# Optimization experiments

Measured on AMD Instinct MI355X. Metric: run time of the kernel, lower is better.

Reference implementation:

```python
import jax, jax.numpy as jnp
import numpy as np

HEAD = 16
EMB = 1024
D_K = EMB // HEAD


def setup_inputs() -> dict:
    key = jax.random.key(0)
    ks = jax.random.split(key, 11)
    B, S, E = 2, 2048, EMB
    scale = 1.0 / np.sqrt(E)
    inp = {
        "query": jax.random.normal(ks[0], (B, S, E), jnp.float32),
        "key": jax.random.normal(ks[1], (B, S, E), jnp.float32),
        "value": jax.random.normal(ks[2], (B, S, E), jnp.float32),
        "Wq": jax.random.normal(ks[3], (E, E), jnp.float32) * scale,
        "bq": jnp.zeros((E,), jnp.float32),
        "Wk": jax.random.normal(ks[4], (E, E), jnp.float32) * scale,
        "bk": jnp.zeros((E,), jnp.float32),
        "Wv": jax.random.normal(ks[5], (E, E), jnp.float32) * scale,
        "bv": jnp.zeros((E,), jnp.float32),
        "Wo": jax.random.normal(ks[6], (E, E), jnp.float32) * scale,
        "bo": jnp.zeros((E,), jnp.float32),
    }
    return inp


def reference(query, key, value, Wq, bq, Wk, bk, Wv, bv, Wo, bo):
    B, S, E = query.shape
    # 3 input projections, split into heads: [B, H, S, d_k]
    def proj(x, W, b):
        return (x @ W.T + b).reshape(B, S, HEAD, D_K).transpose(0, 2, 1, 3)

    q = proj(query, Wq, bq)
    k = proj(key, Wk, bk)
    v = proj(value, Wv, bv)

    # scaled dot-product attention (full matrix, as in original)
    scores = jnp.einsum("bhqd,bhkd->bhqk", q, k) / jnp.sqrt(jnp.float32(D_K))
    attn = jax.nn.softmax(scores, axis=-1)  # dropout in eval mode = identity
    x = jnp.einsum("bhqk,bhkd->bhqd", attn, v)

    # merge heads and output projection
    x = x.transpose(0, 2, 1, 3).reshape(B, S, E)
    return x @ Wo.T + bo
```

## Files before the change

kernel.cpp:

```cpp
#include <hip/hip_runtime.h>
#include <hip/hip_bf16.h>
#include <math.h>


constexpr int Sn = 2048;
constexpr int En = 1024;
constexpr int Hn = 16;
constexpr int Dk = 64;
constexpr int Kn = 1024;
constexpr size_t WSZ = 1048576;
constexpr size_t TSZ = 4194304;

#define QSCALE 0.18033688011112042f

typedef __bf16 bf16x8 __attribute__((ext_vector_type(8)));
typedef float  f32x4  __attribute__((ext_vector_type(4)));
typedef float  f32x16 __attribute__((ext_vector_type(16)));

union U16 { uint4 u; bf16x8 v; __hip_bfloat16 h[8]; };
union U8  { uint2 u; __hip_bfloat162 h2[2]; __hip_bfloat16 h[4]; };
union U4  { unsigned u; __hip_bfloat162 h2; };

__device__ inline U16 cvt8f(const float* __restrict__ p) {
    float4 a = *(const float4*)p;
    float4 b = *(const float4*)(p + 4);
    U16 r;
    r.h[0] = __float2bfloat16(a.x); r.h[1] = __float2bfloat16(a.y);
    r.h[2] = __float2bfloat16(a.z); r.h[3] = __float2bfloat16(a.w);
    r.h[4] = __float2bfloat16(b.x); r.h[5] = __float2bfloat16(b.y);
    r.h[6] = __float2bfloat16(b.z); r.h[7] = __float2bfloat16(b.w);
    return r;
}

__device__ inline void gload16(const __hip_bfloat16* g, __hip_bfloat16* l) {
    __builtin_amdgcn_global_load_lds(
        (const __attribute__((address_space(1))) void*)g,
        (__attribute__((address_space(3))) void*)l, 16, 0, 0);
}

template<int ROWS, int NW>
__device__ inline void stage_tile(const __hip_bfloat16* __restrict__ src, int ld,
                                  __hip_bfloat16* lds, int w, int lane) {
    int l8 = lane >> 3;
    int g = (lane & 7) ^ (l8 & 7);
    #pragma unroll
    for (int j = 0; j < ROWS / (8 * NW); ++j) {
        int c = j * NW + w;
        gload16(src + (size_t)(c * 8 + l8) * ld + g * 8, lds + c * 512);
    }
}

__global__ __launch_bounds__(256)
void cvt_w(const float* __restrict__ w0, const float* __restrict__ w1,
           const float* __restrict__ w2, const float* __restrict__ w3,
           __hip_bfloat16* __restrict__ dst)
{
    int y = blockIdx.y;
    const float* src = (y == 0) ? w0 : (y == 1) ? w1 : (y == 2) ? w2 : w3;
    size_t i = ((size_t)blockIdx.x * 256 + threadIdx.x) * 8;
    U16 r = cvt8f(src + i);
    *(uint4*)&dst[(size_t)y * WSZ + i] = r.u;
}

__global__ __launch_bounds__(256)
void cvt_x3(const float* __restrict__ q, const float* __restrict__ k,
            const float* __restrict__ v, __hip_bfloat16* __restrict__ dst)
{
    int z = blockIdx.y;
    const float* src = (z == 0) ? q : (z == 1) ? k : v;
    size_t i = ((size_t)blockIdx.x * 256 + threadIdx.x) * 8;
    U16 r = cvt8f(src + i);
    *(uint4*)&dst[(size_t)z * TSZ + i] = r.u;
}

template<int NT>
__device__ inline void gemm_core(const __hip_bfloat16* __restrict__ Ab,
                                 const __hip_bfloat16* __restrict__ Wb,
                                 __hip_bfloat16* As, __hip_bfloat16* Bs,
                                 f32x4 (&acc)[2][NT], int w, int lane)
{
    const int l15 = lane & 15, lg = lane >> 4, l7 = lane & 7;
    const int wm = (w & 1) * 32, wn = (w >> 1) * (NT * 16);
    const int coff0 = (lg ^ l7) * 8;
    const int coff1 = ((4 + lg) ^ l7) * 8;

    #pragma unroll
    for (int i = 0; i < 2; ++i)
        #pragma unroll
        for (int j = 0; j < NT; ++j) acc[i][j] = {0.f, 0.f, 0.f, 0.f};

    for (int k0 = 0; k0 < Kn; k0 += 64) {
        stage_tile<64, 4>(Ab + k0, Kn, As, w, lane);
        stage_tile<NT * 32, 4>(Wb + k0, Kn, Bs, w, lane);
        __syncthreads();

        U16 af[2][2], bf[NT][2];
        #pragma unroll
        for (int mt = 0; mt < 2; ++mt) {
            int r = (wm + mt * 16 + l15) * 64;
            af[mt][0].u = *(const uint4*)&As[r + coff0];
            af[mt][1].u = *(const uint4*)&As[r + coff1];
        }
        #pragma unroll
        for (int nt = 0; nt < NT; ++nt) {
            int r = (wn + nt * 16 + l15) * 64;
            bf[nt][0].u = *(const uint4*)&Bs[r + coff0];
            bf[nt][1].u = *(const uint4*)&Bs[r + coff1];
        }
        #pragma unroll
        for (int mt = 0; mt < 2; ++mt)
            #pragma unroll
            for (int nt = 0; nt < NT; ++nt) {
                acc[mt][nt] = __builtin_amdgcn_mfma_f32_16x16x32_bf16(af[mt][0].v, bf[nt][0].v, acc[mt][nt], 0, 0, 0);
                acc[mt][nt] = __builtin_amdgcn_mfma_f32_16x16x32_bf16(af[mt][1].v, bf[nt][1].v, acc[mt][nt], 0, 0, 0);
            }
        __syncthreads();
    }
}

__global__ __launch_bounds__(256)
void gemm_qkv(const __hip_bfloat16* __restrict__ X, const __hip_bfloat16* __restrict__ Wall,
              const float* __restrict__ bq, const float* __restrict__ bk,
              const float* __restrict__ bv, __hip_bfloat16* __restrict__ outbase)
{
    __shared__ __align__(16) __hip_bfloat16 As[64 * 64];
    __shared__ __align__(16) __hip_bfloat16 Bs[128 * 64];

    const int tid = threadIdx.x, w = tid >> 6, lane = tid & 63;
    const int z = blockIdx.z;
    const int blockM = blockIdx.x * 64, blockN = blockIdx.y * 128;

    f32x4 acc[2][4];
    gemm_core<4>(X + (size_t)z * TSZ + (size_t)blockM * Kn,
                 Wall + (size_t)z * WSZ + (size_t)blockN * Kn,
                 As, Bs, acc, w, lane);

    const float scale = (z == 0) ? QSCALE : 1.0f;
    const float* bias = (z == 0) ? bq : (z == 1) ? bk : bv;
    __hip_bfloat16* out = outbase + (size_t)z * TSZ;

    const int l15 = lane & 15, lg = lane >> 4;
    const int wm = (w & 1) * 32, wn = (w >> 1) * 64;

    #pragma unroll
    for (int nt = 0; nt < 4; ++nt) {
        int n = blockN + wn + nt * 16 + l15;
        float bvn = bias[n] * scale;
        int h_ = n >> 6, d_ = n & 63;
        #pragma unroll
        for (int mt = 0; mt < 2; ++mt) {
            int m0 = blockM + wm + mt * 16 + lg * 4;
            int b_ = m0 >> 11, s_ = m0 & (Sn - 1);
            if (z < 2) {
                #pragma unroll
                for (int i = 0; i < 4; ++i)
                    out[(((size_t)b_ * Hn + h_) * Sn + s_ + i) * Dk + d_] =
                        __float2bfloat16(fmaf(acc[mt][nt][i], scale, bvn));
            } else {
                U8 pk;
                #pragma unroll
                for (int i = 0; i < 4; ++i)
                    pk.h[i] = __float2bfloat16(fmaf(acc[mt][nt][i], scale, bvn));
                *(uint2*)&out[(((size_t)b_ * Hn + h_) * Dk + d_) * Sn + s_] = pk.u;
            }
        }
    }
}

__global__ __launch_bounds__(256)
void gemm_out(const __hip_bfloat16* __restrict__ A, const __hip_bfloat16* __restrict__ W,
              const float* __restrict__ bias, float* __restrict__ out)
{
    __shared__ __align__(16) __hip_bfloat16 As[64 * 64];
    __shared__ __align__(16) __hip_bfloat16 Bs[64 * 64];

    const int tid = threadIdx.x, w = tid >> 6, lane = tid & 63;
    const int blockM = blockIdx.x * 64, blockN = blockIdx.y * 64;

    f32x4 acc[2][2];
    gemm_core<2>(A + (size_t)blockM * Kn, W + (size_t)blockN * Kn,
                 As, Bs, acc, w, lane);

    const int l15 = lane & 15, lg = lane >> 4;
    const int wm = (w & 1) * 32, wn = (w >> 1) * 32;

    #pragma unroll
    for (int nt = 0; nt < 2; ++nt) {
        int n = blockN + wn + nt * 16 + l15;
        float bvn = bias[n];
        #pragma unroll
        for (int mt = 0; mt < 2; ++mt) {
            int m0 = blockM + wm + mt * 16 + lg * 4;
            #pragma unroll
            for (int i = 0; i < 4; ++i)
                out[(size_t)(m0 + i) * Kn + n] = acc[mt][nt][i] + bvn;
        }
    }
}

__global__ __launch_bounds__(256)
void attn(const __hip_bfloat16* __restrict__ Q, const __hip_bfloat16* __restrict__ K,
          const __hip_bfloat16* __restrict__ Vt, __hip_bfloat16* __restrict__ X)
{
    __shared__ __align__(16) __hip_bfloat16 Ks[4][64 * 64];
    __shared__ __align__(16) __hip_bfloat16 Vts[4][64 * 64];

    const int bh = blockIdx.y, q0 = blockIdx.x * 128;
    const int tid = threadIdx.x, w = tid >> 6, lane = tid & 63;
    const int l31 = lane & 31, hi = lane >> 5;

    const __hip_bfloat16* Qb = Q  + (size_t)bh * Sn * Dk;
    const __hip_bfloat16* Kb = K  + (size_t)bh * Sn * Dk;
    const __hip_bfloat16* Vb = Vt + (size_t)bh * Dk * Sn;

    U16 qf[4];
    {
        const __hip_bfloat16* qp = Qb + (size_t)(q0 + w * 32 + l31) * Dk + hi * 8;
        #pragma unroll
        for (int d0t = 0; d0t < 4; ++d0t)
            qf[d0t].u = *(const uint4*)(qp + d0t * 16);
    }
    asm volatile("s_waitcnt vmcnt(0)" ::: "memory");

    f32x16 o[2];
    #pragma unroll
    for (int dt = 0; dt < 2; ++dt)
        #pragma unroll
        for (int r = 0; r < 16; ++r) o[dt][r] = 0.f;
    float lpart = 0.f;

    #pragma unroll
    for (int p = 0; p < 3; ++p) {
        stage_tile<64, 4>(Kb + (size_t)p * 64 * Dk, Dk, Ks[p], w, lane);
        stage_tile<64, 4>(Vb + p * 64, Sn, Vts[p], w, lane);
    }

    for (int t = 0; t < Sn / 64; ++t) {
        asm volatile("s_waitcnt vmcnt(8)" ::: "memory");
        __builtin_amdgcn_s_barrier();
        __builtin_amdgcn_sched_barrier(0);

        const int ts = (t + 3) & 31;
        const int sb = (t + 3) & 3;
        stage_tile<64, 4>(Kb + (size_t)ts * 64 * Dk, Dk, Ks[sb], w, lane);
        stage_tile<64, 4>(Vb + ts * 64, Sn, Vts[sb], w, lane);

        const int cur = t & 3;

        f32x16 st[2];
        #pragma unroll
        for (int kt = 0; kt < 2; ++kt)
            #pragma unroll
            for (int r = 0; r < 16; ++r) st[kt][r] = 0.f;

        __builtin_amdgcn_s_setprio(1);
        #pragma unroll
        for (int d0t = 0; d0t < 4; ++d0t) {
            #pragma unroll
            for (int kt = 0; kt < 2; ++kt) {
                int r = kt * 32 + l31;
                int col = (((d0t * 2 + hi)) ^ (r & 7)) * 8;
                U16 kf; kf.u = *(const uint4*)&Ks[cur][r * 64 + col];
                st[kt] = __builtin_amdgcn_mfma_f32_32x32x16_bf16(kf.v, qf[d0t].v, st[kt], 0, 0, 0);
            }
        }
        __builtin_amdgcn_s_setprio(0);

        uint4 pa[4];
        #pragma unroll
        for (int kt = 0; kt < 2; ++kt) {
            float pv[16];
            #pragma unroll
            for (int r = 0; r < 16; ++r) pv[r] = __builtin_amdgcn_exp2f(st[kt][r]);
            float s01 = (pv[0] + pv[1]) + (pv[2] + pv[3]);
            float s23 = (pv[4] + pv[5]) + (pv[6] + pv[7]);
            float s45 = (pv[8] + pv[9]) + (pv[10] + pv[11]);
            float s67 = (pv[12] + pv[13]) + (pv[14] + pv[15]);
            lpart += (s01 + s23) + (s45 + s67);

            uint wv[8];
            #pragma unroll
            for (int m2 = 0; m2 < 8; ++m2) {
                U4 pk; pk.h2 = __float22bfloat162_rn({pv[2 * m2], pv[2 * m2 + 1]});
                wv[m2] = pk.u;
            }
            asm volatile("v_permlane32_swap_b32 %0, %1" : "+v"(wv[0]), "+v"(wv[2]));
            asm volatile("v_permlane32_swap_b32 %0, %1" : "+v"(wv[1]), "+v"(wv[3]));
            asm volatile("v_permlane32_swap_b32 %0, %1" : "+v"(wv[4]), "+v"(wv[6]));
            asm volatile("v_permlane32_swap_b32 %0, %1" : "+v"(wv[5]), "+v"(wv[7]));
            pa[kt * 2 + 0] = make_uint4(wv[0], wv[1], wv[2], wv[3]);
            pa[kt * 2 + 1] = make_uint4(wv[4], wv[5], wv[6], wv[7]);
        }

        __builtin_amdgcn_s_setprio(1);
        #pragma unroll
        for (int k0t = 0; k0t < 4; ++k0t) {
            U16 pau; pau.u = pa[k0t];
            #pragma unroll
            for (int dt = 0; dt < 2; ++dt) {
                int r = dt * 32 + l31;
                int col = (((k0t * 2 + hi)) ^ (r & 7)) * 8;
                U16 vf; vf.u = *(const uint4*)&Vts[cur][r * 64 + col];
                o[dt] = __builtin_amdgcn_mfma_f32_32x32x16_bf16(pau.v, vf.v, o[dt], 0, 0, 0);
            }
        }
        __builtin_amdgcn_s_setprio(0);
    }

    asm volatile("s_waitcnt vmcnt(0)" ::: "memory");

    lpart += __shfl_xor(lpart, 32, 64);
    float linv = 1.f / lpart;

    float li[16];
    #pragma unroll
    for (int r = 0; r < 16; ++r) {
        int qr = (r & 3) + 8 * (r >> 2) + 4 * hi;
        li[r] = __shfl(linv, qr, 64);
    }

    int b_ = bh >> 4, h_ = bh & (Hn - 1);
    #pragma unroll
    for (int r = 0; r < 16; ++r) {
        int qr = (r & 3) + 8 * (r >> 2) + 4 * hi;
        int sr = q0 + w * 32 + qr;
        __hip_bfloat16* xp = X + ((size_t)(b_ * Sn + sr)) * En + h_ * Dk + l31;
        xp[0]  = __float2bfloat16(o[0][r] * li[r]);
        xp[32] = __float2bfloat16(o[1][r] * li[r]);
    }
}

extern "C" void kernel_launch(void* const* d_in, const int* in_sizes, int n_in,
                              void* d_out, int out_size, void* d_ws, size_t ws_size,
                              hipStream_t stream)
{
    const float* query = (const float*)d_in[0];
    const float* key   = (const float*)d_in[1];
    const float* value = (const float*)d_in[2];
    const float* Wq = (const float*)d_in[3];
    const float* bq = (const float*)d_in[4];
    const float* Wk = (const float*)d_in[5];
    const float* bk = (const float*)d_in[6];
    const float* Wv = (const float*)d_in[7];
    const float* bv = (const float*)d_in[8];
    const float* Wo = (const float*)d_in[9];
    const float* bo = (const float*)d_in[10];
    float* out = (float*)d_out;

    __hip_bfloat16* xqkv = (__hip_bfloat16*)d_ws;
    __hip_bfloat16* Wbf  = xqkv + 3 * TSZ;
    __hip_bfloat16* QKVw = Wbf + 4 * WSZ;
    __hip_bfloat16* Xw   = xqkv;

    cvt_w<<<dim3(512, 4), 256, 0, stream>>>(Wq, Wk, Wv, Wo, Wbf);
    cvt_x3<<<dim3(2048, 3), 256, 0, stream>>>(query, key, value, xqkv);
    gemm_qkv<<<dim3(64, 8, 3), 256, 0, stream>>>(xqkv, Wbf, bq, bk, bv, QKVw);
    attn<<<dim3(Sn / 128, 32), 256, 0, stream>>>(QKVw, QKVw + TSZ, QKVw + 2 * TSZ, Xw);
    gemm_out<<<dim3(64, 16), 256, 0, stream>>>(Xw, Wbf + 3 * WSZ, bo, out);
}
```

Before: 237.9 us.

## Split attention KV loop across two wave groups with LDS reduction

Attention blocks grow to 512 threads, and the two 4-wave groups take alternate 64-key tiles. Their partial outputs and row sums are combined through shared memory at the end. The 4-stage prefetch ring becomes a double buffer with __syncthreads, setprio hints are dropped, and the grid is reordered so head index varies fastest. The aim is more waves per block for latency hiding, at the cost of half the waves idling on each iteration, a full barrier per tile, and an extra LDS reduction.

```diff
diff --git a/kernel.cpp b/kernel.cpp
--- a/kernel.cpp
+++ b/kernel.cpp
@@ -198,15 +198,16 @@
     }
 }
 
-__global__ __launch_bounds__(256)
+__global__ __launch_bounds__(512)
 void attn(const __hip_bfloat16* __restrict__ Q, const __hip_bfloat16* __restrict__ K,
           const __hip_bfloat16* __restrict__ Vt, __hip_bfloat16* __restrict__ X)
 {
-    __shared__ __align__(16) __hip_bfloat16 Ks[4][64 * 64];
-    __shared__ __align__(16) __hip_bfloat16 Vts[4][64 * 64];
-
-    const int bh = blockIdx.y, q0 = blockIdx.x * 128;
+    __shared__ __align__(16) __hip_bfloat16 KVs[2][2][64 * 64];
+    __shared__ float Lc[4][64];
+
+    const int bh = blockIdx.x, q0 = blockIdx.y * 128;
     const int tid = threadIdx.x, w = tid >> 6, lane = tid & 63;
+    const int qs = w & 3, g = w >> 2;
     const int l31 = lane & 31, hi = lane >> 5;
 
     const __hip_bfloat16* Qb = Q  + (size_t)bh * Sn * Dk;
@@ -215,12 +216,11 @@
 
     U16 qf[4];
     {
-        const __hip_bfloat16* qp = Qb + (size_t)(q0 + w * 32 + l31) * Dk + hi * 8;
+        const __hip_bfloat16* qp = Qb + (size_t)(q0 + qs * 32 + l31) * Dk + hi * 8;
         #pragma unroll
         for (int d0t = 0; d0t < 4; ++d0t)
             qf[d0t].u = *(const uint4*)(qp + d0t * 16);
     }
-    asm volatile("s_waitcnt vmcnt(0)" ::: "memory");
 
     f32x16 o[2];
     #pragma unroll
@@ -229,23 +229,20 @@
         for (int r = 0; r < 16; ++r) o[dt][r] = 0.f;
     float lpart = 0.f;
 
-    #pragma unroll
-    for (int p = 0; p < 3; ++p) {
-        stage_tile<64, 4>(Kb + (size_t)p * 64 * Dk, Dk, Ks[p], w, lane);
-        stage_tile<64, 4>(Vb + p * 64, Sn, Vts[p], w, lane);
-    }
+    stage_tile<64, 8>(Kb, Dk, KVs[0][0], w, lane);
+    stage_tile<64, 8>(Vb, Sn, KVs[0][1], w, lane);
 
     for (int t = 0; t < Sn / 64; ++t) {
-        asm volatile("s_waitcnt vmcnt(8)" ::: "memory");
-        __builtin_amdgcn_s_barrier();
-        __builtin_amdgcn_sched_barrier(0);
-
-        const int ts = (t + 3) & 31;
-        const int sb = (t + 3) & 3;
-        stage_tile<64, 4>(Kb + (size_t)ts * 64 * Dk, Dk, Ks[sb], w, lane);
-        stage_tile<64, 4>(Vb + ts * 64, Sn, Vts[sb], w, lane);
-
-        const int cur = t & 3;
+        __syncthreads();
+        const int cur = t & 1;
+        if (t + 1 < Sn / 64) {
+            stage_tile<64, 8>(Kb + (size_t)(t + 1) * 64 * Dk, Dk, KVs[cur ^ 1][0], w, lane);
+            stage_tile<64, 8>(Vb + (t + 1) * 64, Sn, KVs[cur ^ 1][1], w, lane);
+        }
+        if (cur != g) continue;
+
+        const __hip_bfloat16* Ksc = KVs[cur][0];
+        const __hip_bfloat16* Vsc = KVs[cur][1];
 
         f32x16 st[2];
         #pragma unroll
@@ -253,18 +250,16 @@
             #pragma unroll
             for (int r = 0; r < 16; ++r) st[kt][r] = 0.f;
 
-        __builtin_amdgcn_s_setprio(1);
         #pragma unroll
         for (int d0t = 0; d0t < 4; ++d0t) {
             #pragma unroll
             for (int kt = 0; kt < 2; ++kt) {
                 int r = kt * 32 + l31;
                 int col = (((d0t * 2 + hi)) ^ (r & 7)) * 8;
-                U16 kf; kf.u = *(const uint4*)&Ks[cur][r * 64 + col];
+                U16 kf; kf.u = *(const uint4*)&Ksc[r * 64 + col];
                 st[kt] = __builtin_amdgcn_mfma_f32_32x32x16_bf16(kf.v, qf[d0t].v, st[kt], 0, 0, 0);
             }
         }
-        __builtin_amdgcn_s_setprio(0);
 
         uint4 pa[4];
         #pragma unroll
@@ -292,7 +287,6 @@
             pa[kt * 2 + 1] = make_uint4(wv[4], wv[5], wv[6], wv[7]);
         }
 
-        __builtin_amdgcn_s_setprio(1);
         #pragma unroll
         for (int k0t = 0; k0t < 4; ++k0t) {
             U16 pau; pau.u = pa[k0t];
@@ -300,33 +294,53 @@
             for (int dt = 0; dt < 2; ++dt) {
                 int r = dt * 32 + l31;
                 int col = (((k0t * 2 + hi)) ^ (r & 7)) * 8;
-                U16 vf; vf.u = *(const uint4*)&Vts[cur][r * 64 + col];
+                U16 vf; vf.u = *(const uint4*)&Vsc[r * 64 + col];
                 o[dt] = __builtin_amdgcn_mfma_f32_32x32x16_bf16(pau.v, vf.v, o[dt], 0, 0, 0);
             }
         }
-        __builtin_amdgcn_s_setprio(0);
-    }
-
-    asm volatile("s_waitcnt vmcnt(0)" ::: "memory");
-
-    lpart += __shfl_xor(lpart, 32, 64);
-    float linv = 1.f / lpart;
-
-    float li[16];
-    #pragma unroll
-    for (int r = 0; r < 16; ++r) {
-        int qr = (r & 3) + 8 * (r >> 2) + 4 * hi;
-        li[r] = __shfl(linv, qr, 64);
-    }
-
-    int b_ = bh >> 4, h_ = bh & (Hn - 1);
-    #pragma unroll
-    for (int r = 0; r < 16; ++r) {
-        int qr = (r & 3) + 8 * (r >> 2) + 4 * hi;
-        int sr = q0 + w * 32 + qr;
-        __hip_bfloat16* xp = X + ((size_t)(b_ * Sn + sr)) * En + h_ * Dk + l31;
-        xp[0]  = __float2bfloat16(o[0][r] * li[r]);
-        xp[32] = __float2bfloat16(o[1][r] * li[r]);
+    }
+
+    __syncthreads();
+    float* Ocomb = (float*)KVs;
+    if (g == 0) {
+        #pragma unroll
+        for (int dt = 0; dt < 2; ++dt)
+            #pragma unroll
+            for (int r = 0; r < 16; ++r) {
+                int qr = (r & 3) + 8 * (r >> 2) + 4 * hi;
+                Ocomb[(qs * 32 + qr) * 64 + dt * 32 + l31] = o[dt][r];
+            }
+        Lc[qs][lane] = lpart;
+    }
+    __syncthreads();
+    if (g == 1) {
+        #pragma unroll
+        for (int dt = 0; dt < 2; ++dt)
+            #pragma unroll
+            for (int r = 0; r < 16; ++r) {
+                int qr = (r & 3) + 8 * (r >> 2) + 4 * hi;
+                o[dt][r] += Ocomb[(qs * 32 + qr) * 64 + dt * 32 + l31];
+            }
+        lpart += Lc[qs][lane];
+        lpart += __shfl_xor(lpart, 32, 64);
+        float linv = 1.f / lpart;
+
+        float li[16];
+        #pragma unroll
+        for (int r = 0; r < 16; ++r) {
+            int qr = (r & 3) + 8 * (r >> 2) + 4 * hi;
+            li[r] = __shfl(linv, qr, 64);
+        }
+
+        int b_ = bh >> 4, h_ = bh & (Hn - 1);
+        #pragma unroll
+        for (int r = 0; r < 16; ++r) {
+            int qr = (r & 3) + 8 * (r >> 2) + 4 * hi;
+            int sr = q0 + qs * 32 + qr;
+            __hip_bfloat16* xp = X + ((size_t)(b_ * Sn + sr)) * En + h_ * Dk + l31;
+            xp[0]  = __float2bfloat16(o[0][r] * li[r]);
+            xp[32] = __float2bfloat16(o[1][r] * li[r]);
+        }
     }
 }
 
@@ -355,6 +369,6 @@
     cvt_w<<<dim3(512, 4), 256, 0, stream>>>(Wq, Wk, Wv, Wo, Wbf);
     cvt_x3<<<dim3(2048, 3), 256, 0, stream>>>(query, key, value, xqkv);
     gemm_qkv<<<dim3(64, 8, 3), 256, 0, stream>>>(xqkv, Wbf, bq, bk, bv, QKVw);
-    attn<<<dim3(Sn / 128, 32), 256, 0, stream>>>(QKVw, QKVw + TSZ, QKVw + 2 * TSZ, Xw);
+    attn<<<dim3(32, Sn / 128), 512, 0, stream>>>(QKVw, QKVw + TSZ, QKVw + 2 * TSZ, Xw);
     gemm_out<<<dim3(64, 16), 256, 0, stream>>>(Xw, Wbf + 3 * WSZ, bo, out);
 }
```

Result: no change. 237.9 us (-0.0%).
